# Kernel tuning notes

Measured on AMD Instinct MI355X. Metric: run time of the kernel, lower is better.

The kernel has to match this reference:

```python
import jax, jax.numpy as jnp
import numpy as np

N, E = 50000, 800000
NF, HC, H, NC = 512, 64, 8, 16
NEG_SLOPE = 0.2


def setup_inputs() -> dict:
    key = jax.random.key(0)
    ks = jax.random.split(key, 10)
    x = jax.random.normal(ks[0], (N, NF), dtype=jnp.float32)
    edge_index = jax.random.randint(ks[1], (2, E), 0, N, dtype=jnp.int64)
    # layer 1 params (GATConv nf -> hc, heads=H, concat)
    w1 = jax.random.normal(ks[2], (NF, H * HC), dtype=jnp.float32) / np.sqrt(NF)
    a_src1 = jax.random.normal(ks[3], (H, HC), dtype=jnp.float32) / np.sqrt(HC)
    a_dst1 = jax.random.normal(ks[4], (H, HC), dtype=jnp.float32) / np.sqrt(HC)
    b1 = jnp.zeros((H * HC,), dtype=jnp.float32)
    # layer 2 params (GATConv hc*h -> nc, heads=1, concat=False)
    w2 = jax.random.normal(ks[5], (H * HC, NC), dtype=jnp.float32) / np.sqrt(H * HC)
    a_src2 = jax.random.normal(ks[6], (1, NC), dtype=jnp.float32) / np.sqrt(NC)
    a_dst2 = jax.random.normal(ks[7], (1, NC), dtype=jnp.float32) / np.sqrt(NC)
    b2 = jnp.zeros((NC,), dtype=jnp.float32)
    return {"x": x, "edge_index": edge_index, "w1": w1, "a_src1": a_src1,
            "a_dst1": a_dst1, "b1": b1, "w2": w2, "a_src2": a_src2,
            "a_dst2": a_dst2, "b2": b2}


def _gat_conv(x, src, dst, W, a_src, a_dst, heads, out_ch):
    # x: [N, F_in] -> h: [N, H, C]
    h = (x @ W).reshape(N, heads, out_ch)
    alpha_src = jnp.einsum('nhc,hc->nh', h, a_src)  # [N, H]
    alpha_dst = jnp.einsum('nhc,hc->nh', h, a_dst)  # [N, H]
    e = jax.nn.leaky_relu(alpha_src[src] + alpha_dst[dst], NEG_SLOPE)  # [E', H]
    # segment-wise softmax over edges grouped by destination node
    m = jax.ops.segment_max(e, dst, num_segments=N)
    ex = jnp.exp(e - m[dst])
    denom = jax.ops.segment_sum(ex, dst, num_segments=N)
    alpha = ex / denom[dst]  # [E', H]
    out = jax.ops.segment_sum(h[src] * alpha[:, :, None], dst, num_segments=N)
    return out  # [N, H, C]


def reference(x, edge_index, w1, a_src1, a_dst1, b1, w2, a_src2, a_dst2, b2):
    # add self loops (PyG GATConv default)
    loops = jnp.arange(N, dtype=edge_index.dtype)
    src = jnp.concatenate([edge_index[0], loops])
    dst = jnp.concatenate([edge_index[1], loops])
    # layer 1: heads concatenated, dropout is identity in eval mode
    emb = _gat_conv(x, src, dst, w1, a_src1, a_dst1, H, HC).reshape(N, H * HC) + b1
    h_act = jax.nn.elu(emb)
    # layer 2: single head, no concat
    logits = _gat_conv(h_act, src, dst, w2, a_src2, a_dst2, 1, NC).reshape(N, NC) + b2
    return (logits, emb)
```

## Files before the change

### kernel.cpp

```cpp
#include <hip/hip_runtime.h>
#include <math.h>

#define N_NODES 50000
#define M_PAD   50048
#define N_EDGES 800000
#define ET (N_EDGES + N_NODES)
#define NF 512
#define HC 64
#define NH 8
#define D1 512
#define NC 16
#define NEG_SLOPE 0.2f

typedef __attribute__((ext_vector_type(8))) short bf16x8;
typedef __attribute__((ext_vector_type(4))) float floatx4;

static __device__ __forceinline__ float b2f(unsigned short u) {
  union { unsigned int i; float f; } v; v.i = ((unsigned int)u) << 16; return v.f;
}
static __device__ __forceinline__ unsigned short f2b(float f) {
  union { float f; unsigned int i; } v; v.f = f;
  unsigned int r = v.i + 0x7fffu + ((v.i >> 16) & 1u);
  return (unsigned short)(r >> 16);
}

static __device__ __forceinline__ void async_cp16(const void* g, void* l) {
  __builtin_amdgcn_global_load_lds(
      (const __attribute__((address_space(1))) unsigned int*)g,
      (__attribute__((address_space(3))) unsigned int*)l, 16, 0, 0);
}

__global__ __launch_bounds__(256) void k_cast_x(const float* __restrict__ x,
                                                unsigned short* __restrict__ xb) {
  size_t i = ((size_t)blockIdx.x * 256 + threadIdx.x) * 8;
  if (i >= (size_t)M_PAD * NF) return;
  int row = (int)(i >> 9);
  union { unsigned short s[8]; uint4 v; } u;
  if (row < N_NODES) {
    float4 v0 = *(const float4*)&x[i];
    float4 v1 = *(const float4*)&x[i + 4];
    u.s[0] = f2b(v0.x); u.s[1] = f2b(v0.y); u.s[2] = f2b(v0.z); u.s[3] = f2b(v0.w);
    u.s[4] = f2b(v1.x); u.s[5] = f2b(v1.y); u.s[6] = f2b(v1.z); u.s[7] = f2b(v1.w);
  } else {
    u.v = make_uint4(0, 0, 0, 0);
  }
  *(uint4*)&xb[i] = u.v;
}

__global__ __launch_bounds__(256) void k_w1t(const float* __restrict__ w1,
                                             unsigned short* __restrict__ w1t) {
  __shared__ float t[32][33];
  int tx = threadIdx.x & 31, ty = threadIdx.x >> 5;
  int k0 = blockIdx.x * 32, n0 = blockIdx.y * 32;
  for (int r = ty; r < 32; r += 8)
    t[r][tx] = w1[(size_t)(k0 + r) * D1 + n0 + tx];
  __syncthreads();
  for (int r = ty; r < 32; r += 8)
    w1t[(size_t)(n0 + r) * NF + k0 + tx] = f2b(t[tx][r]);
}

__global__ __launch_bounds__(256) void k_gemm1m(const unsigned short* __restrict__ xb,
                                                const unsigned short* __restrict__ w1t,
                                                unsigned short* __restrict__ h1b) {
  __shared__ unsigned short As[128 * 32];
  __shared__ unsigned short Bs[128 * 32];
  const int tid  = threadIdx.x;
  const int w    = tid >> 6;
  const int lane = tid & 63;
  const int l16  = lane & 15;
  const int quad = lane >> 4;
  const int bm = blockIdx.y * 128;
  const int bn = blockIdx.x * 128;
  const int wr = (w >> 1) * 64;
  const int wc = (w & 1) * 64;

  floatx4 acc[4][4] = {};

  const int c0 = 2 * w, c1 = 2 * w + 1;
  const unsigned short* ga0 = xb  + (size_t)(bm + c0 * 16 + (lane >> 2)) * NF + (lane & 3) * 8;
  const unsigned short* ga1 = xb  + (size_t)(bm + c1 * 16 + (lane >> 2)) * NF + (lane & 3) * 8;
  const unsigned short* gb0 = w1t + (size_t)(bn + c0 * 16 + (lane >> 2)) * NF + (lane & 3) * 8;
  const unsigned short* gb1 = w1t + (size_t)(bn + c1 * 16 + (lane >> 2)) * NF + (lane & 3) * 8;
  unsigned short* la0 = &As[c0 * 512];
  unsigned short* la1 = &As[c1 * 512];
  unsigned short* lb0 = &Bs[c0 * 512];
  unsigned short* lb1 = &Bs[c1 * 512];

  for (int k0 = 0; k0 < NF; k0 += 32) {
    async_cp16(ga0, la0);
    async_cp16(ga1, la1);
    async_cp16(gb0, lb0);
    async_cp16(gb1, lb1);
    ga0 += 32; ga1 += 32; gb0 += 32; gb1 += 32;
    __syncthreads();
    bf16x8 af[4], bfr[4];
#pragma unroll
    for (int i = 0; i < 4; ++i)
      af[i] = *(const bf16x8*)&As[(wr + i * 16 + l16) * 32 + quad * 8];
#pragma unroll
    for (int j = 0; j < 4; ++j)
      bfr[j] = *(const bf16x8*)&Bs[(wc + j * 16 + l16) * 32 + quad * 8];
#pragma unroll
    for (int i = 0; i < 4; ++i)
#pragma unroll
      for (int j = 0; j < 4; ++j)
        acc[i][j] = __builtin_amdgcn_mfma_f32_16x16x32_bf16(af[i], bfr[j], acc[i][j], 0, 0, 0);
    __syncthreads();
  }

#pragma unroll
  for (int i = 0; i < 4; ++i)
#pragma unroll
    for (int j = 0; j < 4; ++j) {
      int col = bn + wc + j * 16 + l16;
#pragma unroll
      for (int r = 0; r < 4; ++r) {
        int row = bm + wr + i * 16 + quad * 4 + r;
        h1b[(size_t)row * D1 + col] = f2b(acc[i][j][r]);
      }
    }
}

__global__ void k_alphas1(const unsigned short* __restrict__ h1b,
                          const float* __restrict__ a_src,
                          const float* __restrict__ a_dst,
                          float* __restrict__ as1, float* __restrict__ ad1) {
  int i = blockIdx.x * 256 + threadIdx.x;
  if (i >= N_NODES * NH) return;
  int n = i >> 3, hd = i & 7;
  const unsigned short* hp = h1b + (size_t)n * D1 + hd * HC;
  const float* aw = a_src + hd * HC;
  const float* dw = a_dst + hd * HC;
  float s = 0.f, d = 0.f;
#pragma unroll
  for (int c = 0; c < HC; c += 8) {
    bf16x8 hv = *(const bf16x8*)&hp[c];
#pragma unroll
    for (int j = 0; j < 8; ++j) {
      float v = b2f((unsigned short)hv[j]);
      s += v * aw[c + j];
      d += v * dw[c + j];
    }
  }
  as1[i] = s; ad1[i] = d;
}

__global__ void k_degree(const int* __restrict__ ei, int* __restrict__ deg) {
  int i = blockIdx.x * 256 + threadIdx.x;
  if (i >= ET) return;
  int dst = (i < N_EDGES) ? ei[N_EDGES + i] : (i - N_EDGES);
  atomicAdd(&deg[dst], 1);
}

__global__ void k_reduce(const int* __restrict__ deg, int* __restrict__ bsums) {
  __shared__ int s[1024];
  int i = blockIdx.x * 1024 + threadIdx.x;
  s[threadIdx.x] = (i < N_NODES) ? deg[i] : 0;
  __syncthreads();
  for (int off = 512; off > 0; off >>= 1) {
    if (threadIdx.x < off) s[threadIdx.x] += s[threadIdx.x + off];
    __syncthreads();
  }
  if (threadIdx.x == 0) bsums[blockIdx.x] = s[0];
}

__global__ void k_scan_small(int* __restrict__ bsums, int nb) {
  int lane = threadIdx.x;
  int v = (lane < nb) ? bsums[lane] : 0;
  int orig = v;
  for (int off = 1; off < 64; off <<= 1) {
    int u = __shfl_up(v, off);
    if (lane >= off) v += u;
  }
  __syncthreads();
  if (lane < nb) bsums[lane] = v - orig;
}

__global__ void k_scan_final(const int* __restrict__ deg,
                             const int* __restrict__ bsums_ex,
                             int* __restrict__ rowp, int* __restrict__ pos) {
  __shared__ int s[1024];
  int i = blockIdx.x * 1024 + threadIdx.x;
  int v = (i < N_NODES) ? deg[i] : 0;
  s[threadIdx.x] = v;
  __syncthreads();
  for (int off = 1; off < 1024; off <<= 1) {
    int t = (threadIdx.x >= off) ? s[threadIdx.x - off] : 0;
    __syncthreads();
    s[threadIdx.x] += t;
    __syncthreads();
  }
  int inc = s[threadIdx.x];
  int ex  = inc - v + bsums_ex[blockIdx.x];
  if (i < N_NODES) { rowp[i] = ex; pos[i] = ex; }
  if (i == N_NODES - 1) rowp[N_NODES] = ex + v;
}

__global__ void k_scatter(const int* __restrict__ ei, int* __restrict__ pos,
                          int* __restrict__ csr) {
  int i = blockIdx.x * 256 + threadIdx.x;
  if (i >= ET) return;
  int s, d;
  if (i < N_EDGES) { s = ei[i]; d = ei[N_EDGES + i]; }
  else             { s = d = i - N_EDGES; }
  int slot = atomicAdd(&pos[d], 1);
  csr[slot] = s;
}

static __device__ __forceinline__ void ld_edge1(const unsigned short* __restrict__ h1b,
                                                const float* __restrict__ as1,
                                                int src, int head, int col,
                                                bf16x8& hv, float& al) {
  al = as1[src * NH + head];
  hv = *(const bf16x8*)&h1b[(size_t)src * D1 + col];
}

static __device__ __forceinline__ void use_edge1(const bf16x8& hv, float al, float adv,
                                                 float& den, float acc[8]) {
  float e = al + adv;
  e = (e >= 0.f) ? e : NEG_SLOPE * e;
  float wgt = __expf(e);
  den += wgt;
#pragma unroll
  for (int jj = 0; jj < 8; ++jj) acc[jj] += wgt * b2f((unsigned short)hv[jj]);
}

__global__ __launch_bounds__(256) void k_agg1(const unsigned short* __restrict__ h1b,
                                              const float* __restrict__ as1,
                                              const float* __restrict__ ad1,
                                              const int* __restrict__ rowp,
                                              const int* __restrict__ csr,
                                              const float* __restrict__ b1,
                                              float* __restrict__ emb) {
  const int wid  = threadIdx.x >> 6;
  const int lane = threadIdx.x & 63;
  const int node = blockIdx.x * 4 + wid;
  if (node >= N_NODES) return;
  const int start = rowp[node], end = rowp[node + 1];
  const int head = lane >> 3;
  const int col  = lane * 8;
  const float adv = ad1[node * NH + head];

  bf16x8 h0, h1, h2, h3;
  float  a0, a1, a2, a3;

  {
    int i0 = csr[start];
    int i1 = (start + 1 < end) ? csr[start + 1] : 0;
    int i2 = (start + 2 < end) ? csr[start + 2] : 0;
    int i3 = (start + 3 < end) ? csr[start + 3] : 0;
    ld_edge1(h1b, as1, i0, head, col, h0, a0);
    if (start + 1 < end) ld_edge1(h1b, as1, i1, head, col, h1, a1);
    if (start + 2 < end) ld_edge1(h1b, as1, i2, head, col, h2, a2);
    if (start + 3 < end) ld_edge1(h1b, as1, i3, head, col, h3, a3);
  }

  float den = 0.f;
  float acc[8] = {};
  for (int j = start; j < end; j += 4) {
    int n0 = (j + 4 < end) ? csr[j + 4] : 0;
    int n1 = (j + 5 < end) ? csr[j + 5] : 0;
    int n2 = (j + 6 < end) ? csr[j + 6] : 0;
    int n3 = (j + 7 < end) ? csr[j + 7] : 0;
    use_edge1(h0, a0, adv, den, acc);
    if (j + 4 < end) ld_edge1(h1b, as1, n0, head, col, h0, a0);
    if (j + 1 < end) use_edge1(h1, a1, adv, den, acc);
    if (j + 5 < end) ld_edge1(h1b, as1, n1, head, col, h1, a1);
    if (j + 2 < end) use_edge1(h2, a2, adv, den, acc);
    if (j + 6 < end) ld_edge1(h1b, as1, n2, head, col, h2, a2);
    if (j + 3 < end) use_edge1(h3, a3, adv, den, acc);
    if (j + 7 < end) ld_edge1(h1b, as1, n3, head, col, h3, a3);
  }
  const float rden = 1.f / den;

  const float4 bb0 = *(const float4*)&b1[col];
  const float4 bb1 = *(const float4*)&b1[col + 4];
  float4 o0 = make_float4(acc[0] * rden + bb0.x, acc[1] * rden + bb0.y,
                          acc[2] * rden + bb0.z, acc[3] * rden + bb0.w);
  float4 o1 = make_float4(acc[4] * rden + bb1.x, acc[5] * rden + bb1.y,
                          acc[6] * rden + bb1.z, acc[7] * rden + bb1.w);
  *(float4*)&emb[(size_t)node * D1 + col]     = o0;
  *(float4*)&emb[(size_t)node * D1 + col + 4] = o1;
}

static __device__ __forceinline__ void split_bf16(float x, unsigned short& h,
                                                  unsigned short& l) {
  h = f2b(x);
  float rem = x - b2f(h);
  l = f2b(rem);
}

__global__ __launch_bounds__(256) void k_gemm2m(const float* __restrict__ emb,
                                                const float* __restrict__ W2,
                                                const float* __restrict__ a_src2,
                                                const float* __restrict__ a_dst2,
                                                float* __restrict__ h2,
                                                float* __restrict__ as2,
                                                float* __restrict__ ad2) {
  const int wv   = threadIdx.x >> 6;
  const int lane = threadIdx.x & 63;
  const int l16  = lane & 15;
  const int quad = lane >> 4;
  const int n0 = blockIdx.x * 128 + wv * 32 + l16;
  const int n1 = n0 + 16;
  const bool v0 = n0 < N_NODES, v1 = n1 < N_NODES;

  floatx4 acc0 = {0.f, 0.f, 0.f, 0.f};
  floatx4 acc1 = {0.f, 0.f, 0.f, 0.f};

  const float* e0 = emb + (size_t)n0 * D1 + quad * 8;
  const float* e1 = emb + (size_t)n1 * D1 + quad * 8;
  const float* wp = W2 + (size_t)(quad * 8) * NC + l16;

#pragma unroll 2
  for (int kk = 0; kk < D1; kk += 32) {
    bf16x8 ah, al;
#pragma unroll
    for (int j = 0; j < 8; ++j) {
      float wv2 = wp[(size_t)(kk + j) * NC];
      unsigned short h, l;
      split_bf16(wv2, h, l);
      ah[j] = (short)h; al[j] = (short)l;
    }
    bf16x8 bh0, bl0, bh1, bl1;
    {
      float4 pa = v0 ? *(const float4*)&e0[kk] : make_float4(0.f, 0.f, 0.f, 0.f);
      float4 pb = v0 ? *(const float4*)&e0[kk + 4] : make_float4(0.f, 0.f, 0.f, 0.f);
      float t[8] = {pa.x, pa.y, pa.z, pa.w, pb.x, pb.y, pb.z, pb.w};
#pragma unroll
      for (int j = 0; j < 8; ++j) {
        float xx = t[j];
        float s = (xx > 0.f) ? xx : (__expf(xx) - 1.f);
        unsigned short h, l;
        split_bf16(s, h, l);
        bh0[j] = (short)h; bl0[j] = (short)l;
      }
    }
    {
      float4 pa = v1 ? *(const float4*)&e1[kk] : make_float4(0.f, 0.f, 0.f, 0.f);
      float4 pb = v1 ? *(const float4*)&e1[kk + 4] : make_float4(0.f, 0.f, 0.f, 0.f);
      float t[8] = {pa.x, pa.y, pa.z, pa.w, pb.x, pb.y, pb.z, pb.w};
#pragma unroll
      for (int j = 0; j < 8; ++j) {
        float xx = t[j];
        float s = (xx > 0.f) ? xx : (__expf(xx) - 1.f);
        unsigned short h, l;
        split_bf16(s, h, l);
        bh1[j] = (short)h; bl1[j] = (short)l;
      }
    }
    acc0 = __builtin_amdgcn_mfma_f32_16x16x32_bf16(ah, bh0, acc0, 0, 0, 0);
    acc0 = __builtin_amdgcn_mfma_f32_16x16x32_bf16(ah, bl0, acc0, 0, 0, 0);
    acc0 = __builtin_amdgcn_mfma_f32_16x16x32_bf16(al, bh0, acc0, 0, 0, 0);
    acc1 = __builtin_amdgcn_mfma_f32_16x16x32_bf16(ah, bh1, acc1, 0, 0, 0);
    acc1 = __builtin_amdgcn_mfma_f32_16x16x32_bf16(ah, bl1, acc1, 0, 0, 0);
    acc1 = __builtin_amdgcn_mfma_f32_16x16x32_bf16(al, bh1, acc1, 0, 0, 0);
  }

  const float4 asv = ((const float4*)a_src2)[quad];
  const float4 adv = ((const float4*)a_dst2)[quad];
  float sa0 = acc0[0] * asv.x + acc0[1] * asv.y + acc0[2] * asv.z + acc0[3] * asv.w;
  float da0 = acc0[0] * adv.x + acc0[1] * adv.y + acc0[2] * adv.z + acc0[3] * adv.w;
  float sa1 = acc1[0] * asv.x + acc1[1] * asv.y + acc1[2] * asv.z + acc1[3] * asv.w;
  float da1 = acc1[0] * adv.x + acc1[1] * adv.y + acc1[2] * adv.z + acc1[3] * adv.w;
  sa0 += __shfl_xor(sa0, 16); sa0 += __shfl_xor(sa0, 32);
  da0 += __shfl_xor(da0, 16); da0 += __shfl_xor(da0, 32);
  sa1 += __shfl_xor(sa1, 16); sa1 += __shfl_xor(sa1, 32);
  da1 += __shfl_xor(da1, 16); da1 += __shfl_xor(da1, 32);

  if (v0) {
    *(float4*)&h2[(size_t)n0 * NC + quad * 4] =
        make_float4(acc0[0], acc0[1], acc0[2], acc0[3]);
    if (quad == 0) { as2[n0] = sa0; ad2[n0] = da0; }
  }
  if (v1) {
    *(float4*)&h2[(size_t)n1 * NC + quad * 4] =
        make_float4(acc1[0], acc1[1], acc1[2], acc1[3]);
    if (quad == 0) { as2[n1] = sa1; ad2[n1] = da1; }
  }
}

__global__ __launch_bounds__(256) void k_agg2(const float* __restrict__ h2,
                                              const float* __restrict__ as2,
                                              const float* __restrict__ ad2,
                                              const int* __restrict__ rowp,
                                              const int* __restrict__ csr,
                                              const float* __restrict__ b2,
                                              float* __restrict__ logits) {
  const int wid  = threadIdx.x >> 6;
  const int lane = threadIdx.x & 63;
  const int node = blockIdx.x * 4 + wid;
  if (node >= N_NODES) return;
  const int start = rowp[node], end = rowp[node + 1];
  const float adv = ad2[node];
  const int g = lane >> 4;
  const int c = lane & 15;

  int jA = start + g;
  int sA = (jA < end) ? csr[jA] : -1;
  int jB = jA + 4;
  int sB = (jB < end) ? csr[jB] : -1;
  float eA = 0.f, vA = 0.f;
  if (sA >= 0) { eA = as2[sA]; vA = h2[(size_t)sA * NC + c]; }

  float den = 0.f, acc = 0.f;
  for (int base = start; base < end; base += 4) {
    float eB = 0.f, vB = 0.f;
    if (sB >= 0) { eB = as2[sB]; vB = h2[(size_t)sB * NC + c]; }
    int jC = base + 8 + g;
    int sC = (jC < end) ? csr[jC] : -1;
    if (sA >= 0) {
      float e = eA + adv;
      e = (e >= 0.f) ? e : NEG_SLOPE * e;
      float wgt = __expf(e);
      den += wgt;
      acc += wgt * vA;
    }
    sA = sB; eA = eB; vA = vB; sB = sC;
  }
  acc += __shfl_xor(acc, 16); acc += __shfl_xor(acc, 32);
  den += __shfl_xor(den, 16); den += __shfl_xor(den, 32);
  if (lane < 16) logits[(size_t)node * NC + lane] = acc / den + b2[lane];
}

extern "C" void kernel_launch(void* const* d_in, const int* in_sizes, int n_in,
                              void* d_out, int out_size, void* d_ws, size_t ws_size,
                              hipStream_t stream) {
  const float* x      = (const float*)d_in[0];
  const int*   ei     = (const int*)d_in[1];
  const float* w1     = (const float*)d_in[2];
  const float* a_src1 = (const float*)d_in[3];
  const float* a_dst1 = (const float*)d_in[4];
  const float* b1     = (const float*)d_in[5];
  const float* w2     = (const float*)d_in[6];
  const float* a_src2 = (const float*)d_in[7];
  const float* a_dst2 = (const float*)d_in[8];
  const float* b2     = (const float*)d_in[9];

  char* w = (char*)d_ws;
  char* xb_region = w;
  unsigned short* xb  = (unsigned short*)w; w += (size_t)M_PAD * NF * 2;
  unsigned short* h1b = (unsigned short*)w; w += (size_t)M_PAD * D1 * 2;
  unsigned short* w1t = (unsigned short*)w; w += (size_t)NF * D1 * 2;
  float* as1 = (float*)w;  w += (size_t)N_NODES * NH * 4;
  float* ad1 = (float*)w;  w += (size_t)N_NODES * NH * 4;
  int* deg   = (int*)w;    w += (size_t)N_NODES * 4;
  int* rowp  = (int*)w;    w += (size_t)50064 * 4;
  int* pos   = (int*)w;    w += (size_t)N_NODES * 4;
  int* csr   = (int*)w;    w += (size_t)ET * 4;
  int* bsums = (int*)w;    w += 256;
  float* h2  = (float*)xb_region;
  float* as2 = (float*)(xb_region + (size_t)N_NODES * NC * 4);
  float* ad2 = (float*)(xb_region + (size_t)N_NODES * NC * 4 + (size_t)N_NODES * 4);

  float* logits = (float*)d_out;
  float* emb    = (float*)d_out + (size_t)N_NODES * NC;

  hipMemsetAsync(deg, 0, N_NODES * sizeof(int), stream);

  k_cast_x<<<(int)(((size_t)M_PAD * NF / 8 + 255) / 256), 256, 0, stream>>>(x, xb);
  k_w1t<<<dim3(16, 16), 256, 0, stream>>>(w1, w1t);
  k_gemm1m<<<dim3(4, M_PAD / 128), 256, 0, stream>>>(xb, w1t, h1b);
  k_alphas1<<<(N_NODES * NH + 255) / 256, 256, 0, stream>>>(h1b, a_src1, a_dst1, as1, ad1);

  k_degree<<<(ET + 255) / 256, 256, 0, stream>>>(ei, deg);
  k_reduce<<<49, 1024, 0, stream>>>(deg, bsums);
  k_scan_small<<<1, 64, 0, stream>>>(bsums, 49);
  k_scan_final<<<49, 1024, 0, stream>>>(deg, bsums, rowp, pos);
  k_scatter<<<(ET + 255) / 256, 256, 0, stream>>>(ei, pos, csr);

  k_agg1<<<(N_NODES + 3) / 4, 256, 0, stream>>>(h1b, as1, ad1, rowp, csr, b1, emb);

  k_gemm2m<<<(N_NODES + 127) / 128, 256, 0, stream>>>(emb, w2, a_src2, a_dst2, h2, as2, ad2);
  k_agg2<<<(N_NODES + 3) / 4, 256, 0, stream>>>(h2, as2, ad2, rowp, csr, b2, logits);
}
```

Measured before the change: 549.8 us.

## Fuse fp32-to-bf16 cast into layer-1 GEMM with full-width tiles and double-buffered B

Removes the separate kernel that casts x to bf16 and instead has the layer-1 GEMM read fp32 x directly, converting to bf16 in registers before staging into LDS. Each 512-thread block now computes a full 128x512 output row tile, so x is read only once instead of once per column tile, and the W1 tiles are double-buffered with async global-to-LDS copies. Nontemporal loads and stores are also applied to the CSR index reads, the emb write and the emb read in the layer-2 GEMM, to reduce cache pollution. The larger accumulator set (32 floatx4 per thread) raises register pressure and may reduce occupancy.

```diff
diff --git a/kernel.cpp b/kernel.cpp
--- a/kernel.cpp
+++ b/kernel.cpp
@@ -30,23 +30,6 @@
       (__attribute__((address_space(3))) unsigned int*)l, 16, 0, 0);
 }
 
-__global__ __launch_bounds__(256) void k_cast_x(const float* __restrict__ x,
-                                                unsigned short* __restrict__ xb) {
-  size_t i = ((size_t)blockIdx.x * 256 + threadIdx.x) * 8;
-  if (i >= (size_t)M_PAD * NF) return;
-  int row = (int)(i >> 9);
-  union { unsigned short s[8]; uint4 v; } u;
-  if (row < N_NODES) {
-    float4 v0 = *(const float4*)&x[i];
-    float4 v1 = *(const float4*)&x[i + 4];
-    u.s[0] = f2b(v0.x); u.s[1] = f2b(v0.y); u.s[2] = f2b(v0.z); u.s[3] = f2b(v0.w);
-    u.s[4] = f2b(v1.x); u.s[5] = f2b(v1.y); u.s[6] = f2b(v1.z); u.s[7] = f2b(v1.w);
-  } else {
-    u.v = make_uint4(0, 0, 0, 0);
-  }
-  *(uint4*)&xb[i] = u.v;
-}
-
 __global__ __launch_bounds__(256) void k_w1t(const float* __restrict__ w1,
                                              unsigned short* __restrict__ w1t) {
   __shared__ float t[32][33];
@@ -59,63 +42,83 @@
     w1t[(size_t)(n0 + r) * NF + k0 + tx] = f2b(t[tx][r]);
 }
 
-__global__ __launch_bounds__(256) void k_gemm1m(const unsigned short* __restrict__ xb,
+__global__ __launch_bounds__(512) void k_gemm1f(const float* __restrict__ x,
                                                 const unsigned short* __restrict__ w1t,
                                                 unsigned short* __restrict__ h1b) {
   __shared__ unsigned short As[128 * 32];
-  __shared__ unsigned short Bs[128 * 32];
+  __shared__ unsigned short Bs[2][512 * 32];
   const int tid  = threadIdx.x;
   const int w    = tid >> 6;
   const int lane = tid & 63;
   const int l16  = lane & 15;
   const int quad = lane >> 4;
-  const int bm = blockIdx.y * 128;
-  const int bn = blockIdx.x * 128;
-  const int wr = (w >> 1) * 64;
-  const int wc = (w & 1) * 64;
-
-  floatx4 acc[4][4] = {};
-
-  const int c0 = 2 * w, c1 = 2 * w + 1;
-  const unsigned short* ga0 = xb  + (size_t)(bm + c0 * 16 + (lane >> 2)) * NF + (lane & 3) * 8;
-  const unsigned short* ga1 = xb  + (size_t)(bm + c1 * 16 + (lane >> 2)) * NF + (lane & 3) * 8;
-  const unsigned short* gb0 = w1t + (size_t)(bn + c0 * 16 + (lane >> 2)) * NF + (lane & 3) * 8;
-  const unsigned short* gb1 = w1t + (size_t)(bn + c1 * 16 + (lane >> 2)) * NF + (lane & 3) * 8;
-  unsigned short* la0 = &As[c0 * 512];
-  unsigned short* la1 = &As[c1 * 512];
-  unsigned short* lb0 = &Bs[c0 * 512];
-  unsigned short* lb1 = &Bs[c1 * 512];
-
-  for (int k0 = 0; k0 < NF; k0 += 32) {
-    async_cp16(ga0, la0);
-    async_cp16(ga1, la1);
-    async_cp16(gb0, lb0);
-    async_cp16(gb1, lb1);
-    ga0 += 32; ga1 += 32; gb0 += 32; gb1 += 32;
+  const int bm   = blockIdx.x * 128;
+  const int wr   = (w >> 1) * 32;
+  const int wc   = (w & 1) * 256;
+
+  const int arow = tid >> 2;
+  const int acg  = tid & 3;
+  const bool aval = (bm + arow) < N_NODES;
+  const float* agp = x + (size_t)(bm + arow) * NF + acg * 8;
+
+  const int bn_base = w * 16 + (lane >> 2);
+  const int bko     = (lane & 3) * 8;
+
+  floatx4 acc[2][16] = {};
+  floatx4 ar0 = {0.f, 0.f, 0.f, 0.f}, ar1 = {0.f, 0.f, 0.f, 0.f};
+
+#pragma unroll
+  for (int r = 0; r < 4; ++r) {
+    const int n = r * 128 + bn_base;
+    async_cp16(w1t + (size_t)n * NF + bko, &Bs[0][n * 32 + bko]);
+  }
+  if (aval) {
+    ar0 = __builtin_nontemporal_load((const floatx4*)agp);
+    ar1 = __builtin_nontemporal_load((const floatx4*)(agp + 4));
+  }
+
+  for (int s = 0; s < NF / 32; ++s) {
+    const int cur = s & 1;
+    bf16x8 av;
+    av[0] = (short)f2b(ar0[0]); av[1] = (short)f2b(ar0[1]);
+    av[2] = (short)f2b(ar0[2]); av[3] = (short)f2b(ar0[3]);
+    av[4] = (short)f2b(ar1[0]); av[5] = (short)f2b(ar1[1]);
+    av[6] = (short)f2b(ar1[2]); av[7] = (short)f2b(ar1[3]);
+    *(bf16x8*)&As[arow * 32 + acg * 8] = av;
     __syncthreads();
-    bf16x8 af[4], bfr[4];
-#pragma unroll
-    for (int i = 0; i < 4; ++i)
-      af[i] = *(const bf16x8*)&As[(wr + i * 16 + l16) * 32 + quad * 8];
-#pragma unroll
-    for (int j = 0; j < 4; ++j)
-      bfr[j] = *(const bf16x8*)&Bs[(wc + j * 16 + l16) * 32 + quad * 8];
-#pragma unroll
-    for (int i = 0; i < 4; ++i)
-#pragma unroll
-      for (int j = 0; j < 4; ++j)
-        acc[i][j] = __builtin_amdgcn_mfma_f32_16x16x32_bf16(af[i], bfr[j], acc[i][j], 0, 0, 0);
+
+    if (s + 1 < NF / 32) {
+      const int kk1 = (s + 1) * 32;
+#pragma unroll
+      for (int r = 0; r < 4; ++r) {
+        const int n = r * 128 + bn_base;
+        async_cp16(w1t + (size_t)n * NF + kk1 + bko, &Bs[cur ^ 1][n * 32 + bko]);
+      }
+      if (aval) {
+        ar0 = __builtin_nontemporal_load((const floatx4*)(agp + kk1));
+        ar1 = __builtin_nontemporal_load((const floatx4*)(agp + kk1 + 4));
+      }
+    }
+
+    bf16x8 af0 = *(const bf16x8*)&As[(wr + l16) * 32 + quad * 8];
+    bf16x8 af1 = *(const bf16x8*)&As[(wr + 16 + l16) * 32 + quad * 8];
+#pragma unroll
+    for (int j = 0; j < 16; ++j) {
+      bf16x8 bf = *(const bf16x8*)&Bs[cur][(wc + j * 16 + l16) * 32 + quad * 8];
+      acc[0][j] = __builtin_amdgcn_mfma_f32_16x16x32_bf16(af0, bf, acc[0][j], 0, 0, 0);
+      acc[1][j] = __builtin_amdgcn_mfma_f32_16x16x32_bf16(af1, bf, acc[1][j], 0, 0, 0);
+    }
     __syncthreads();
   }
 
 #pragma unroll
-  for (int i = 0; i < 4; ++i)
-#pragma unroll
-    for (int j = 0; j < 4; ++j) {
-      int col = bn + wc + j * 16 + l16;
+  for (int i = 0; i < 2; ++i)
+#pragma unroll
+    for (int j = 0; j < 16; ++j) {
+      const int col = wc + j * 16 + l16;
 #pragma unroll
       for (int r = 0; r < 4; ++r) {
-        int row = bm + wr + i * 16 + quad * 4 + r;
+        const int row = bm + wr + i * 16 + quad * 4 + r;
         h1b[(size_t)row * D1 + col] = f2b(acc[i][j][r]);
       }
     }
@@ -245,10 +248,10 @@
   float  a0, a1, a2, a3;
 
   {
-    int i0 = csr[start];
-    int i1 = (start + 1 < end) ? csr[start + 1] : 0;
-    int i2 = (start + 2 < end) ? csr[start + 2] : 0;
-    int i3 = (start + 3 < end) ? csr[start + 3] : 0;
+    int i0 = __builtin_nontemporal_load(&csr[start]);
+    int i1 = (start + 1 < end) ? __builtin_nontemporal_load(&csr[start + 1]) : 0;
+    int i2 = (start + 2 < end) ? __builtin_nontemporal_load(&csr[start + 2]) : 0;
+    int i3 = (start + 3 < end) ? __builtin_nontemporal_load(&csr[start + 3]) : 0;
     ld_edge1(h1b, as1, i0, head, col, h0, a0);
     if (start + 1 < end) ld_edge1(h1b, as1, i1, head, col, h1, a1);
     if (start + 2 < end) ld_edge1(h1b, as1, i2, head, col, h2, a2);
@@ -258,10 +261,10 @@
   float den = 0.f;
   float acc[8] = {};
   for (int j = start; j < end; j += 4) {
-    int n0 = (j + 4 < end) ? csr[j + 4] : 0;
-    int n1 = (j + 5 < end) ? csr[j + 5] : 0;
-    int n2 = (j + 6 < end) ? csr[j + 6] : 0;
-    int n3 = (j + 7 < end) ? csr[j + 7] : 0;
+    int n0 = (j + 4 < end) ? __builtin_nontemporal_load(&csr[j + 4]) : 0;
+    int n1 = (j + 5 < end) ? __builtin_nontemporal_load(&csr[j + 5]) : 0;
+    int n2 = (j + 6 < end) ? __builtin_nontemporal_load(&csr[j + 6]) : 0;
+    int n3 = (j + 7 < end) ? __builtin_nontemporal_load(&csr[j + 7]) : 0;
     use_edge1(h0, a0, adv, den, acc);
     if (j + 4 < end) ld_edge1(h1b, as1, n0, head, col, h0, a0);
     if (j + 1 < end) use_edge1(h1, a1, adv, den, acc);
@@ -275,12 +278,12 @@
 
   const float4 bb0 = *(const float4*)&b1[col];
   const float4 bb1 = *(const float4*)&b1[col + 4];
-  float4 o0 = make_float4(acc[0] * rden + bb0.x, acc[1] * rden + bb0.y,
-                          acc[2] * rden + bb0.z, acc[3] * rden + bb0.w);
-  float4 o1 = make_float4(acc[4] * rden + bb1.x, acc[5] * rden + bb1.y,
-                          acc[6] * rden + bb1.z, acc[7] * rden + bb1.w);
-  *(float4*)&emb[(size_t)node * D1 + col]     = o0;
-  *(float4*)&emb[(size_t)node * D1 + col + 4] = o1;
+  floatx4 o0 = {acc[0] * rden + bb0.x, acc[1] * rden + bb0.y,
+                acc[2] * rden + bb0.z, acc[3] * rden + bb0.w};
+  floatx4 o1 = {acc[4] * rden + bb1.x, acc[5] * rden + bb1.y,
+                acc[6] * rden + bb1.z, acc[7] * rden + bb1.w};
+  __builtin_nontemporal_store(o0, (floatx4*)&emb[(size_t)node * D1 + col]);
+  __builtin_nontemporal_store(o1, (floatx4*)&emb[(size_t)node * D1 + col + 4]);
 }
 
 static __device__ __forceinline__ void split_bf16(float x, unsigned short& h,
@@ -324,9 +327,12 @@
     }
     bf16x8 bh0, bl0, bh1, bl1;
     {
-      float4 pa = v0 ? *(const float4*)&e0[kk] : make_float4(0.f, 0.f, 0.f, 0.f);
-      float4 pb = v0 ? *(const float4*)&e0[kk + 4] : make_float4(0.f, 0.f, 0.f, 0.f);
-      float t[8] = {pa.x, pa.y, pa.z, pa.w, pb.x, pb.y, pb.z, pb.w};
+      floatx4 pa = {0.f, 0.f, 0.f, 0.f}, pb = {0.f, 0.f, 0.f, 0.f};
+      if (v0) {
+        pa = __builtin_nontemporal_load((const floatx4*)&e0[kk]);
+        pb = __builtin_nontemporal_load((const floatx4*)&e0[kk + 4]);
+      }
+      float t[8] = {pa[0], pa[1], pa[2], pa[3], pb[0], pb[1], pb[2], pb[3]};
 #pragma unroll
       for (int j = 0; j < 8; ++j) {
         float xx = t[j];
@@ -337,9 +343,12 @@
       }
     }
     {
-      float4 pa = v1 ? *(const float4*)&e1[kk] : make_float4(0.f, 0.f, 0.f, 0.f);
-      float4 pb = v1 ? *(const float4*)&e1[kk + 4] : make_float4(0.f, 0.f, 0.f, 0.f);
-      float t[8] = {pa.x, pa.y, pa.z, pa.w, pb.x, pb.y, pb.z, pb.w};
+      floatx4 pa = {0.f, 0.f, 0.f, 0.f}, pb = {0.f, 0.f, 0.f, 0.f};
+      if (v1) {
+        pa = __builtin_nontemporal_load((const floatx4*)&e1[kk]);
+        pb = __builtin_nontemporal_load((const floatx4*)&e1[kk + 4]);
+      }
+      float t[8] = {pa[0], pa[1], pa[2], pa[3], pb[0], pb[1], pb[2], pb[3]};
 #pragma unroll
       for (int j = 0; j < 8; ++j) {
         float xx = t[j];
@@ -439,7 +448,7 @@
 
   char* w = (char*)d_ws;
   char* xb_region = w;
-  unsigned short* xb  = (unsigned short*)w; w += (size_t)M_PAD * NF * 2;
+  w += (size_t)M_PAD * NF * 2;
   unsigned short* h1b = (unsigned short*)w; w += (size_t)M_PAD * D1 * 2;
   unsigned short* w1t = (unsigned short*)w; w += (size_t)NF * D1 * 2;
   float* as1 = (float*)w;  w += (size_t)N_NODES * NH * 4;
@@ -458,9 +467,8 @@
 
   hipMemsetAsync(deg, 0, N_NODES * sizeof(int), stream);
 
-  k_cast_x<<<(int)(((size_t)M_PAD * NF / 8 + 255) / 256), 256, 0, stream>>>(x, xb);
   k_w1t<<<dim3(16, 16), 256, 0, stream>>>(w1, w1t);
-  k_gemm1m<<<dim3(4, M_PAD / 128), 256, 0, stream>>>(xb, w1t, h1b);
+  k_gemm1f<<<M_PAD / 128, 512, 0, stream>>>(x, w1t, h1b);
   k_alphas1<<<(N_NODES * NH + 255) / 256, 256, 0, stream>>>(h1b, a_src1, a_dst1, as1, ad1);
 
   k_degree<<<(ET + 255) / 256, 256, 0, stream>>>(ei, deg);
```

Result: no change. 550.5 us (+0.1%).
